# Optimization experiments

Hardware: AMD Instinct MI355X
Metric: run time of the kernel (lower is better)

Reference implementation:

```python
import jax, jax.numpy as jnp
import numpy as np

S = 8    # number of path-segments
U = 32   # per-segment input width (subscript 'u')
V = 32   # per-segment output width (subscript 'v')
C = 32   # number of weight groups (indexed dimension)
Z = 65536  # number of rows


def setup_inputs() -> dict:
    key = jax.random.key(0)
    k1, k2, k3 = jax.random.split(key, 3)
    input1 = jax.random.normal(k1, (C, S * U * V), dtype=jnp.float32) * 0.05  # grouped weights
    input2 = jax.random.normal(k2, (Z, S * U), dtype=jnp.float32)             # row features
    counts = jnp.full((C,), Z // C, dtype=jnp.int32)                          # rows per group, contiguous
    coefficients = jax.random.uniform(k3, (S,), dtype=jnp.float32, minval=0.5, maxval=1.5)
    return {"input1": input1, "input2": input2, "counts": counts, "coefficients": coefficients}


def reference(input1, input2, counts, coefficients):
    # Segment-indexed grouped linear: rows are contiguous per group (sizes = counts).
    # For each path-segment s: out_s[z, v] = coeff_s * sum_u x_s[z, u] * W_s[g(z), u, v]
    # Final output concatenates the S segment outputs along the last dim.
    seg_ids = jnp.repeat(jnp.arange(C, dtype=jnp.int32), counts, total_repeat_length=Z)  # [Z]
    outs = []
    for s in range(S):
        W = input1[:, s * U * V:(s + 1) * U * V].reshape(C, U, V)  # [C,U,V]
        x = input2[:, s * U:(s + 1) * U]                           # [Z,U]
        Wz = W[seg_ids]                                            # [Z,U,V] gather by group
        outs.append(coefficients[s] * jnp.einsum('zu,zuv->zv', x, Wz))
    return jnp.concatenate(outs, axis=-1)  # [Z, S*V]
```

## Files before the change

### kernel.cpp

```cpp
#include <hip/hip_runtime.h>


constexpr int S = 8, U = 32, V = 32, C = 32, Z = 65536;
constexpr int SU = S * U;
constexpr int SV = S * V;
constexpr int NT = 256;
constexpr int BZ = 32;
constexpr int TPB = 4;

typedef float    f4     __attribute__((ext_vector_type(4)));
typedef float    f32x16 __attribute__((ext_vector_type(16)));
typedef short    bf16x8 __attribute__((ext_vector_type(8)));
typedef unsigned u32x4  __attribute__((ext_vector_type(4)));

__device__ __forceinline__ unsigned cvtpk(float lo, float hi) {
  unsigned r;
  asm("v_cvt_pk_bf16_f32 %0, %1, %2" : "=v"(r) : "v"(lo), "v"(hi));
  return r;
}

__device__ __forceinline__ short f2bf(float f) {
  unsigned u = __builtin_bit_cast(unsigned, f);
  u = (u + 0x7FFFu + ((u >> 16) & 1u)) >> 16;
  return (short)u;
}

#define LOADX(dst, zt)                                                        \
  do {                                                                        \
    const f4* Xr_ = (const f4*)X + (size_t)((zt) + m) * (SU / 4) + 2 * h;     \
    dst[0] = Xr_[c0 + 0];  dst[1] = Xr_[c0 + 1];                              \
    dst[2] = Xr_[c0 + 4];  dst[3] = Xr_[c0 + 5];                              \
    dst[4] = Xr_[c0 + 8];  dst[5] = Xr_[c0 + 9];                              \
    dst[6] = Xr_[c0 + 12]; dst[7] = Xr_[c0 + 13];                             \
  } while (0)

__global__ __launch_bounds__(NT) void IndexedLinear_kernel(
    const float* __restrict__ W_all,
    const float* __restrict__ X,
    const int*   __restrict__ counts,
    const float* __restrict__ coeff,
    float*       __restrict__ out)
{
  const int tid  = threadIdx.x;
  const int lane = tid & 63;
  const int w    = tid >> 6;
  const int zb   = blockIdx.x * (BZ * TPB);

  const int m  = lane & 31;
  const int h  = lane >> 5;
  const int s0 = 2 * w;
  const int c0 = s0 * 8;

  f4 xA[8], xB[8];
  LOADX(xA, zb);

  int cnt = (lane < C) ? counts[lane] : 0;
  int inc = cnt;
  #pragma unroll
  for (int d = 1; d < 32; d <<= 1) {
    int o = __shfl_up(inc, d, 64);
    if (lane >= d) inc += o;
  }
  const int exc = inc - cnt;

  int curseg = -1;
  u32x4 b1[2], b2[2];

  #pragma unroll
  for (int t = 0; t < TPB; ++t) {
    f4* cur = (t & 1) ? xB : xA;
    f4* nxt = (t & 1) ? xA : xB;
    const int z0 = zb + t * BZ;

    if (t + 1 < TPB) LOADX(nxt, z0 + BZ);

    const unsigned long long ma = __ballot(lane < C && exc <= z0);
    const unsigned long long mb = __ballot(lane < C && exc <= z0 + BZ - 1);
    const int segA = __popcll(ma) - 1;
    const int segB = __popcll(mb) - 1;
    const bool uni = (segA == segB);

    if (uni) {
      if (segA != curseg) {
        curseg = segA;
        const float* wseg = W_all + (size_t)segA * (S * U * V);
        #pragma unroll
        for (int tt = 0; tt < 2; ++tt) {
          const int s = s0 + tt;
          const float cs = coeff[s];
          const float* wb = wseg + s * (U * V) + m;
          #pragma unroll
          for (int j = 0; j < 4; ++j) {
            b1[tt][j] = cvtpk(wb[(8 * h + 2 * j) * V] * cs,
                              wb[(8 * h + 2 * j + 1) * V] * cs);
            b2[tt][j] = cvtpk(wb[(16 + 8 * h + 2 * j) * V] * cs,
                              wb[(16 + 8 * h + 2 * j + 1) * V] * cs);
          }
        }
      }

      #pragma unroll
      for (int tt = 0; tt < 2; ++tt) {
        const int s = s0 + tt;
        const f4 xa = cur[4 * tt + 0], xb = cur[4 * tt + 1];
        const f4 xc = cur[4 * tt + 2], xd = cur[4 * tt + 3];
        u32x4 pa, pb;
        pa[0] = cvtpk(xa[0], xa[1]); pa[1] = cvtpk(xa[2], xa[3]);
        pa[2] = cvtpk(xb[0], xb[1]); pa[3] = cvtpk(xb[2], xb[3]);
        pb[0] = cvtpk(xc[0], xc[1]); pb[1] = cvtpk(xc[2], xc[3]);
        pb[2] = cvtpk(xd[0], xd[1]); pb[3] = cvtpk(xd[2], xd[3]);
        const bf16x8 a1 = __builtin_bit_cast(bf16x8, pa);
        const bf16x8 a2 = __builtin_bit_cast(bf16x8, pb);
        f32x16 acc = {};
        acc = __builtin_amdgcn_mfma_f32_32x32x16_bf16(
            a1, __builtin_bit_cast(bf16x8, b1[tt]), acc, 0, 0, 0);
        acc = __builtin_amdgcn_mfma_f32_32x32x16_bf16(
            a2, __builtin_bit_cast(bf16x8, b2[tt]), acc, 0, 0, 0);

        float* ob = out + (size_t)z0 * SV + s * V + m;
        #pragma unroll
        for (int r = 0; r < 16; ++r) {
          const int row = (r & 3) + 8 * (r >> 2) + 4 * h;
          __builtin_nontemporal_store(acc[r], ob + (size_t)row * SV);
        }
      }
    } else {
      const int zz = z0 + m;
      int sg = 0;
      #pragma unroll 1
      for (int i = 1; i < C; ++i) {
        const int pi = __shfl(exc, i, 64);
        if (pi <= zz) sg = i;
      }
      #pragma unroll 1
      for (int tt = 0; tt < 2; ++tt) {
        const int s = s0 + tt;
        const float cs = coeff[s];
        const float* wr = W_all + (size_t)sg * (S * U * V) + s * (U * V) + 16 * h;
        float accv[16] = {};
        #pragma unroll 1
        for (int cq = 0; cq < 8; ++cq) {
          const f4 xv = ((const f4*)X)[(size_t)zz * (SU / 4) + s * 8 + cq];
          #pragma unroll
          for (int ii = 0; ii < 4; ++ii) {
            const int u = cq * 4 + ii;
            const float xu = xv[ii];
            #pragma unroll
            for (int j = 0; j < 16; ++j) accv[j] += xu * wr[u * V + j];
          }
        }
        float* ob = out + (size_t)zz * SV + s * V + 16 * h;
        #pragma unroll
        for (int j = 0; j < 16; ++j) ob[j] = accv[j] * cs;
      }
    }
  }
}

extern "C" void kernel_launch(void* const* d_in, const int* in_sizes, int n_in,
                              void* d_out, int out_size, void* d_ws, size_t ws_size,
                              hipStream_t stream) {
  const float* input1       = (const float*)d_in[0];
  const float* input2       = (const float*)d_in[1];
  const int*   counts       = (const int*)d_in[2];
  const float* coefficients = (const float*)d_in[3];
  float*       out          = (float*)d_out;

  const int grid = Z / (BZ * TPB);
  IndexedLinear_kernel<<<grid, NT, 0, stream>>>(input1, input2, counts,
                                                coefficients, out);
}
```

Before: 119.1 us.

## Stage X tiles through LDS via async global_load_lds with swizzled double buffering

Replaces the per-lane register double-buffering of X rows with asynchronous global-to-LDS loads (global_load_lds, 16 bytes per lane). The rows are laid out in LDS with an XOR swizzle and double-buffered per wave, and manual s_waitcnt vmcnt counts gate each tile. The aim is fully coalesced row loads and fewer registers held in flight, so more memory-level parallelism overlaps the MFMA work. It adds LDS reads and relies on hand-tuned vmcnt values, which are fragile if the count of outstanding loads changes (for example the weight loads on a segment switch).

```diff
diff --git a/kernel.cpp b/kernel.cpp
--- a/kernel.cpp
+++ b/kernel.cpp
@@ -13,26 +13,14 @@
 typedef short    bf16x8 __attribute__((ext_vector_type(8)));
 typedef unsigned u32x4  __attribute__((ext_vector_type(4)));
 
+typedef const __attribute__((address_space(1))) unsigned gu32;
+typedef __attribute__((address_space(3))) unsigned lu32;
+
 __device__ __forceinline__ unsigned cvtpk(float lo, float hi) {
   unsigned r;
   asm("v_cvt_pk_bf16_f32 %0, %1, %2" : "=v"(r) : "v"(lo), "v"(hi));
   return r;
 }
-
-__device__ __forceinline__ short f2bf(float f) {
-  unsigned u = __builtin_bit_cast(unsigned, f);
-  u = (u + 0x7FFFu + ((u >> 16) & 1u)) >> 16;
-  return (short)u;
-}
-
-#define LOADX(dst, zt)                                                        \
-  do {                                                                        \
-    const f4* Xr_ = (const f4*)X + (size_t)((zt) + m) * (SU / 4) + 2 * h;     \
-    dst[0] = Xr_[c0 + 0];  dst[1] = Xr_[c0 + 1];                              \
-    dst[2] = Xr_[c0 + 4];  dst[3] = Xr_[c0 + 5];                              \
-    dst[4] = Xr_[c0 + 8];  dst[5] = Xr_[c0 + 9];                              \
-    dst[6] = Xr_[c0 + 12]; dst[7] = Xr_[c0 + 13];                             \
-  } while (0)
 
 __global__ __launch_bounds__(NT) void IndexedLinear_kernel(
     const float* __restrict__ W_all,
@@ -49,10 +37,24 @@
   const int m  = lane & 31;
   const int h  = lane >> 5;
   const int s0 = 2 * w;
-  const int c0 = s0 * 8;
+  const int c0 = 16 * w;
+  const int mx = m & 7;
 
-  f4 xA[8], xB[8];
-  LOADX(xA, zb);
+  __shared__ f4 XL[4 * 2 * 512];
+  const int wbase = w * 1024;
+
+  const int rg = lane >> 4;
+  const int ci = lane & 15;
+
+  #pragma unroll
+  for (int k = 0; k < 8; ++k) {
+    const int r  = 4 * k + rg;
+    const int cc = ci ^ (r & 7);
+    const char* gp = (const char*)X
+        + ((size_t)(zb + r) * SU + (c0 + cc) * 4) * 4;
+    __builtin_amdgcn_global_load_lds((gu32*)gp, (lu32*)&XL[wbase + k * 64],
+                                     16, 0, 0);
+  }
 
   int cnt = (lane < C) ? counts[lane] : 0;
   int inc = cnt;
@@ -68,11 +70,25 @@
 
   #pragma unroll
   for (int t = 0; t < TPB; ++t) {
-    f4* cur = (t & 1) ? xB : xA;
-    f4* nxt = (t & 1) ? xA : xB;
     const int z0 = zb + t * BZ;
+    const int bs = wbase + (t & 1) * 512;
 
-    if (t + 1 < TPB) LOADX(nxt, z0 + BZ);
+    if (t + 1 < TPB) {
+      const int nb = wbase + ((t + 1) & 1) * 512;
+      #pragma unroll
+      for (int k = 0; k < 8; ++k) {
+        const int r  = 4 * k + rg;
+        const int cc = ci ^ (r & 7);
+        const char* gp = (const char*)X
+            + ((size_t)(z0 + BZ + r) * SU + (c0 + cc) * 4) * 4;
+        __builtin_amdgcn_global_load_lds((gu32*)gp, (lu32*)&XL[nb + k * 64],
+                                         16, 0, 0);
+      }
+    }
+
+    if (t == 0)            asm volatile("s_waitcnt vmcnt(8)" ::: "memory");
+    else if (t < TPB - 1)  asm volatile("s_waitcnt vmcnt(40)" ::: "memory");
+    else                   asm volatile("s_waitcnt vmcnt(32)" ::: "memory");
 
     const unsigned long long ma = __ballot(lane < C && exc <= z0);
     const unsigned long long mb = __ballot(lane < C && exc <= z0 + BZ - 1);
@@ -102,8 +118,11 @@
       #pragma unroll
       for (int tt = 0; tt < 2; ++tt) {
         const int s = s0 + tt;
-        const f4 xa = cur[4 * tt + 0], xb = cur[4 * tt + 1];
-        const f4 xc = cur[4 * tt + 2], xd = cur[4 * tt + 3];
+        const int cb = tt * 8 + 2 * h;
+        const f4 xa = XL[bs + 16 * m + ((cb + 0) ^ mx)];
+        const f4 xb = XL[bs + 16 * m + ((cb + 1) ^ mx)];
+        const f4 xc = XL[bs + 16 * m + ((cb + 4) ^ mx)];
+        const f4 xd = XL[bs + 16 * m + ((cb + 5) ^ mx)];
         u32x4 pa, pb;
         pa[0] = cvtpk(xa[0], xa[1]); pa[1] = cvtpk(xa[2], xa[3]);
         pa[2] = cvtpk(xb[0], xb[1]); pa[3] = cvtpk(xb[2], xb[3]);
```

New measurement: 118.3 us. No clear change (-0.7%).
